# Kernel tuning notes

Measured on AMD Instinct MI355X. Metric: run time of the kernel, lower is better.

The kernel has to match this reference:

```python
import jax, jax.numpy as jnp
import numpy as np

B, S, H, E, K, NH = 2, 2048, 1024, 8, 2, 8
HD = H // NH          # head dim = 128
HQ = H // 4           # seasonal encoder width = 256
CAP = int(B * S * 1.5 * K / E)  # expert capacity = 1536


def setup_inputs() -> dict:
    key = jax.random.key(0)
    ks = iter(jax.random.split(key, 32))

    def lin(shape):
        fan_in = shape[0]
        return jax.random.normal(next(ks), shape, jnp.float32) / np.sqrt(fan_in)

    inp = {
        "hidden_states": jax.random.normal(next(ks), (B, S, H), jnp.float32),
        # position embedding table [sequence_length, H]
        "pos_emb": jax.random.normal(next(ks), (S, H), jnp.float32) * 0.02,
        # temporal_encoder: Linear(H+2,H) -> ReLU -> Linear(H,H)
        "We1": lin((H + 2, H)), "be1": jnp.zeros((H,), jnp.float32),
        "We2": lin((H, H)),     "be2": jnp.zeros((H,), jnp.float32),
        # seasonal_encoder: Linear(1,H//4) -> ReLU -> Linear(H//4,H//4)
        "Ws1": lin((1, HQ)),   "bs1": jnp.zeros((HQ,), jnp.float32),
        "Ws2": lin((HQ, HQ)),  "bs2": jnp.zeros((HQ,), jnp.float32),
        # temporal_attention (MultiheadAttention, 8 heads)
        "Wq": lin((H, H)), "bq": jnp.zeros((H,), jnp.float32),
        "Wk": lin((H, H)), "bk": jnp.zeros((H,), jnp.float32),
        "Wv": lin((H, H)), "bv": jnp.zeros((H,), jnp.float32),
        "Wo": lin((H, H)), "bo": jnp.zeros((H,), jnp.float32),
        # temporal_router: Linear(H,H) -> ReLU -> Linear(H,E)
        "Wr1": lin((H, H)), "br1": jnp.zeros((H,), jnp.float32),
        "Wr2": lin((H, E)), "br2": jnp.zeros((E,), jnp.float32),
    }
    return inp


def _forward(hidden_states, pos_emb, We1, be1, We2, be2, Ws1, bs1, Ws2, bs2,
             Wq, bq, Wk, bk, Wv, bv, Wo, bo, Wr1, br1, Wr2, br2):
    b, s, h = hidden_states.shape
    # time features (time_info is None -> defaults)
    t = jnp.arange(s, dtype=jnp.float32)                   # [S]
    season = jnp.sin(t * 2.0 * jnp.pi / 24.0)              # [S]
    time_feat = jnp.broadcast_to(jnp.stack([t, season], -1), (b, s, 2))

    combined = jnp.concatenate([hidden_states, time_feat], axis=-1)  # [B,S,H+2]
    enc = jax.nn.relu(combined @ We1 + be1) @ We2 + be2              # [B,S,H]

    pos = pos_emb[:s]                                                # [S,H]
    seas = jax.nn.relu(season[:, None] @ Ws1 + bs1) @ Ws2 + bs2      # [S,H//4]
    seas_full = jnp.tile(seas, (1, h // seas.shape[-1]))             # [S,H] (expand to H)

    x = enc + pos[None] + seas_full[None]                            # [B,S,H]

    # self-attention (eval mode, no dropout)
    def heads(y):
        return y.reshape(b, s, NH, HD)
    q = heads(x @ Wq + bq)
    k = heads(x @ Wk + bk)
    v = heads(x @ Wv + bv)
    scores = jnp.einsum('bqhd,bkhd->bhqk', q, k) / np.sqrt(HD)
    attn = jax.nn.softmax(scores, axis=-1)
    ctx = jnp.einsum('bhqk,bkhd->bqhd', attn, v).reshape(b, s, h)
    x = ctx @ Wo + bo

    logits = jax.nn.relu(x @ Wr1 + br1) @ Wr2 + br2                  # [B,S,E]
    probs = jax.nn.softmax(logits, axis=-1)

    topv, topi = jax.lax.top_k(probs, K)                             # [B,S,K]
    topv = topv / topv.sum(-1, keepdims=True)

    onehot = jax.nn.one_hot(topi, E, dtype=probs.dtype)              # [B,S,K,E]
    disp0 = onehot.sum(-2)                                           # [B,S,E] (0/1)
    comb0 = (topv[..., None] * onehot).sum(-2)                       # [B,S,E]

    # only capacity slot 0 is ever written (per original code)
    dispatch = jnp.zeros((b, s, E, CAP), probs.dtype).at[..., 0].set(disp0)
    combine = jnp.zeros((b, s, E, CAP), probs.dtype).at[..., 0].set(comb0)

    p_mean = probs.mean(axis=(0, 1))                                 # [E]
    aux_loss = jnp.sum(p_mean * jnp.log(p_mean * E + 1e-9))
    return dispatch, combine, probs, aux_loss


def reference(hidden_states, pos_emb, We1, be1, We2, be2, Ws1, bs1, Ws2, bs2,
              Wq, bq, Wk, bk, Wv, bv, Wo, bo, Wr1, br1, Wr2, br2):
    return _forward(hidden_states, pos_emb, We1, be1, We2, be2, Ws1, bs1, Ws2, bs2,
                    Wq, bq, Wk, bk, Wv, bv, Wo, bo, Wr1, br1, Wr2, br2)
```

## Files before the change

### kernel.cpp

```cpp
#include <hip/hip_runtime.h>
#include <hip/hip_fp16.h>
#include <math.h>

#define N_TOK 4096
#define S_LEN 2048
#define H_DIM 1024
#define E_EXP 8
#define CAPV  1536
#define NHEAD 8
#define HDHD  128

typedef __attribute__((ext_vector_type(8))) _Float16 v8h;
typedef __attribute__((ext_vector_type(4))) float v4f;

__device__ __forceinline__ void splitf16(float v, unsigned short& h, unsigned short& l) {
    __half hh = __float2half(v);
    h = __half_as_ushort(hh);
    l = __half_as_ushort(__float2half(v - __half2float(hh)));
}

__device__ __forceinline__ void gld_lds16(const void* g, void* l) {
    __builtin_amdgcn_global_load_lds(
        (const __attribute__((address_space(1))) unsigned int*)g,
        (__attribute__((address_space(3))) unsigned int*)l,
        16, 0, 0);
}

__global__ __launch_bounds__(256) void prep_k(
    const float* __restrict__ hid, unsigned short* __restrict__ hi,
    unsigned short* __restrict__ lo,
    const float* __restrict__ Ws1, const float* __restrict__ bs1,
    const float* __restrict__ Ws2, const float* __restrict__ bs2,
    float* __restrict__ seasons, float* __restrict__ seas24,
    const float* __restrict__ Wr2, float* __restrict__ wr2t) {
    __shared__ float hbuf[256];
    int blk = blockIdx.x;
    int tid = threadIdx.x;
    if (blk < 4096) {
        int i = blk * 256 + tid;
        float4 v = ((const float4*)hid)[i];
        ushort4 h, l;
        splitf16(v.x, h.x, l.x);
        splitf16(v.y, h.y, l.y);
        splitf16(v.z, h.z, l.z);
        splitf16(v.w, h.w, l.w);
        ((ushort4*)hi)[i] = h;
        ((ushort4*)lo)[i] = l;
    } else if (blk < 4104) {
        int s = (blk - 4096) * 256 + tid;
        if (s < S_LEN) {
            double a = (double)s * 2.0 * M_PI / 24.0;
            seasons[s] = (float)sin(a);
        }
    } else if (blk < 4128) {
        int m = blk - 4104;
        double a = (double)m * 2.0 * M_PI / 24.0;
        float sv = (float)sin(a);
        int j = tid;
        hbuf[j] = fmaxf(sv * Ws1[j] + bs1[j], 0.f);
        __syncthreads();
        float acc = bs2[j];
        for (int i = 0; i < 256; ++i) acc = fmaf(hbuf[i], Ws2[i * 256 + j], acc);
        seas24[m * 256 + j] = acc;
    } else {
        int i = (blk - 4128) * 256 + tid;
        int k = i >> 3, e = i & 7;
        wr2t[e * 1024 + k] = Wr2[i];
    }
}

__device__ __forceinline__ void wconv_body(const float* __restrict__ W,
                                           unsigned short* __restrict__ Thi,
                                           unsigned short* __restrict__ Tlo) {
    __shared__ unsigned short Hs[64][65];
    __shared__ unsigned short Ls[64][65];
    int k0 = blockIdx.y * 64, n0 = blockIdx.x * 64;
    int tid = threadIdx.x;
#pragma unroll
    for (int i = 0; i < 4; ++i) {
        int idx = tid + i * 256;
        int kk = idx >> 4, n4 = idx & 15;
        float4 v = *(const float4*)(W + (size_t)(k0 + kk) * 1024 + n0 + n4 * 4);
        unsigned short h, l;
        splitf16(v.x, h, l); Hs[n4 * 4 + 0][kk] = h; Ls[n4 * 4 + 0][kk] = l;
        splitf16(v.y, h, l); Hs[n4 * 4 + 1][kk] = h; Ls[n4 * 4 + 1][kk] = l;
        splitf16(v.z, h, l); Hs[n4 * 4 + 2][kk] = h; Ls[n4 * 4 + 2][kk] = l;
        splitf16(v.w, h, l); Hs[n4 * 4 + 3][kk] = h; Ls[n4 * 4 + 3][kk] = l;
    }
    __syncthreads();
#pragma unroll
    for (int i = 0; i < 4; ++i) {
        int idx = tid + i * 256;
        int n = idx >> 4, k4 = idx & 15;
        ushort4 h = make_ushort4(Hs[n][k4 * 4], Hs[n][k4 * 4 + 1], Hs[n][k4 * 4 + 2], Hs[n][k4 * 4 + 3]);
        ushort4 l = make_ushort4(Ls[n][k4 * 4], Ls[n][k4 * 4 + 1], Ls[n][k4 * 4 + 2], Ls[n][k4 * 4 + 3]);
        *(ushort4*)(Thi + (size_t)(n0 + n) * 1024 + k0 + k4 * 4) = h;
        *(ushort4*)(Tlo + (size_t)(n0 + n) * 1024 + k0 + k4 * 4) = l;
    }
}

__global__ __launch_bounds__(256) void wconv_t_k(const float* __restrict__ W,
                                                 unsigned short* __restrict__ Thi,
                                                 unsigned short* __restrict__ Tlo) {
    wconv_body(W, Thi, Tlo);
}

struct WBatch {
    const float* src[7];
    unsigned short* dh[7];
    unsigned short* dl[7];
};

__global__ __launch_bounds__(256) void wconv_batch_k(WBatch wb) {
    int i = blockIdx.z;
    wconv_body(wb.src[i], wb.dh[i], wb.dl[i]);
}

template <int MODE, int EMITF, int EMITS, int EMITT>
__global__ __launch_bounds__(256, 2) void gemm_split(
    const unsigned short* __restrict__ Ahi, const unsigned short* __restrict__ Alo,
    const unsigned short* __restrict__ WThi, const unsigned short* __restrict__ WTlo,
    const float* __restrict__ bias, float* __restrict__ Cf,
    unsigned short* __restrict__ Chi, unsigned short* __restrict__ Clo,
    const float* __restrict__ rowT, const float* __restrict__ rowS,
    const float* __restrict__ seasons, const float* __restrict__ pos,
    const float* __restrict__ seas24, float escale) {
    __shared__ unsigned short Ash[2][128 * 32];
    __shared__ unsigned short Asl[2][128 * 32];
    __shared__ unsigned short Bsh[2][64 * 32];
    __shared__ unsigned short Bsl[2][64 * 32];
    int tid = threadIdx.x;
    int lane = tid & 63, w = tid >> 6;
    int l15 = lane & 15, l16 = lane >> 4;
    int wm = (w >> 1) * 64, wn = (w & 1) * 32;

    int bid = blockIdx.x;
    int mp = (bid & 7) + ((bid >> 7) << 3);
    int np = (bid >> 3) & 15;
    int m0 = mp * 128, n0 = np * 64;

    int ac0 = w * 128 + lane;
    int ac1 = ac0 + 64;
    int bc  = w * 64 + lane;
    int ar0 = ac0 >> 2, ar1 = ac1 >> 2, bn = bc >> 2;
    size_t a_src0 = (size_t)(m0 + ar0) * 1024 + (((ac0 & 3) ^ (ar0 & 3)) * 8);
    size_t a_src1 = (size_t)(m0 + ar1) * 1024 + (((ac1 & 3) ^ (ar1 & 3)) * 8);
    size_t b_src  = (size_t)(n0 + bn) * 1024 + (((bc & 3) ^ (bn & 3)) * 8);

    int a_off[4], b_off[2];
#pragma unroll
    for (int mi = 0; mi < 4; ++mi) {
        int row = wm + mi * 16 + l15;
        a_off[mi] = row * 32 + ((l16 ^ (row & 3)) * 8);
    }
#pragma unroll
    for (int ni = 0; ni < 2; ++ni) {
        int n = wn + ni * 16 + l15;
        b_off[ni] = n * 32 + ((l16 ^ (n & 3)) * 8);
    }

    auto STAGE = [&](int buf, int k0) {
        gld_lds16(Ahi + a_src0 + k0, &Ash[buf][ac0 * 8]);
        gld_lds16(Ahi + a_src1 + k0, &Ash[buf][ac1 * 8]);
        gld_lds16(Alo + a_src0 + k0, &Asl[buf][ac0 * 8]);
        gld_lds16(Alo + a_src1 + k0, &Asl[buf][ac1 * 8]);
        gld_lds16(WThi + b_src + k0, &Bsh[buf][bc * 8]);
        gld_lds16(WTlo + b_src + k0, &Bsl[buf][bc * 8]);
    };

    v4f acc[4][2] = {};
    STAGE(0, 0);
    __syncthreads();

    for (int kk = 0; kk < 32; ++kk) {
        int cur = kk & 1;
        if (kk < 31) STAGE(cur ^ 1, (kk + 1) * 32);
        v8h ah[4], al[4], bh[2], bl[2];
#pragma unroll
        for (int mi = 0; mi < 4; ++mi) {
            ah[mi] = *(const v8h*)&Ash[cur][a_off[mi]];
            al[mi] = *(const v8h*)&Asl[cur][a_off[mi]];
        }
#pragma unroll
        for (int ni = 0; ni < 2; ++ni) {
            bh[ni] = *(const v8h*)&Bsh[cur][b_off[ni]];
            bl[ni] = *(const v8h*)&Bsl[cur][b_off[ni]];
        }
#pragma unroll
        for (int mi = 0; mi < 4; ++mi)
#pragma unroll
            for (int ni = 0; ni < 2; ++ni) {
                acc[mi][ni] = __builtin_amdgcn_mfma_f32_16x16x32_f16(ah[mi], bh[ni], acc[mi][ni], 0, 0, 0);
                acc[mi][ni] = __builtin_amdgcn_mfma_f32_16x16x32_f16(al[mi], bh[ni], acc[mi][ni], 0, 0, 0);
                acc[mi][ni] = __builtin_amdgcn_mfma_f32_16x16x32_f16(ah[mi], bl[ni], acc[mi][ni], 0, 0, 0);
            }
        __syncthreads();
    }

    if (EMITT) {
#pragma unroll
        for (int mi = 0; mi < 4; ++mi) {
            int row0 = m0 + wm + mi * 16 + l16 * 4;
            int bb = row0 >> 11, ss = row0 & 2047;
#pragma unroll
            for (int ni = 0; ni < 2; ++ni) {
                int col = n0 + wn + ni * 16 + l15;
                int hh = col >> 7, dd = col & 127;
                size_t base = ((size_t)((bb * 8 + hh) * 128 + dd)) * 2048 + ss;
                ushort4 vh, vl;
                float v0 = acc[mi][ni][0] + bias[col];
                float v1 = acc[mi][ni][1] + bias[col];
                float v2 = acc[mi][ni][2] + bias[col];
                float v3 = acc[mi][ni][3] + bias[col];
                splitf16(v0, vh.x, vl.x);
                splitf16(v1, vh.y, vl.y);
                splitf16(v2, vh.z, vl.z);
                splitf16(v3, vh.w, vl.w);
                *(ushort4*)(Chi + base) = vh;
                *(ushort4*)(Clo + base) = vl;
            }
        }
    } else {
#pragma unroll
        for (int mi = 0; mi < 4; ++mi) {
#pragma unroll
            for (int r = 0; r < 4; ++r) {
                int row = m0 + wm + mi * 16 + l16 * 4 + r;
                int s = row & (S_LEN - 1);
                float tval = 0.f, seval = 0.f;
                if (MODE == 1) { tval = (float)s; seval = seasons[s]; }
#pragma unroll
                for (int ni = 0; ni < 2; ++ni) {
                    int col = n0 + wn + ni * 16 + l15;
                    float v = acc[mi][ni][r] + bias[col];
                    if (MODE == 1) v += tval * rowT[col] + seval * rowS[col];
                    if (MODE == 2) v += pos[(size_t)s * 1024 + col] + seas24[(s % 24) * 256 + (col & 255)];
                    if (MODE == 1 || MODE == 3) v = fmaxf(v, 0.f);
                    size_t o = (size_t)row * 1024 + col;
                    if (EMITF) Cf[o] = v;
                    if (EMITS) {
                        unsigned short hu, lu;
                        splitf16(v * escale, hu, lu);
                        Chi[o] = hu; Clo[o] = lu;
                    }
                }
            }
        }
    }
}

__global__ __launch_bounds__(256, 4) void attn_mfma_k(
    const unsigned short* __restrict__ qhi, const unsigned short* __restrict__ qlo,
    const unsigned short* __restrict__ khi, const unsigned short* __restrict__ klo,
    const unsigned short* __restrict__ vthi, const unsigned short* __restrict__ vtlo,
    float* __restrict__ OP, float* __restrict__ ML) {
    __shared__ unsigned short Ks_hi[32 * 128];
    __shared__ unsigned short Ks_lo[32 * 128];
    __shared__ unsigned short Vs_hi[128 * 32];
    __shared__ unsigned short Vs_lo[128 * 32];
    __shared__ unsigned int   Ps[64 * 32];

    int p = blockIdx.x;
    int x = (p >> 3) & 31;
    int g = (p & 7) + ((p >> 8) << 3);
    int bh = g >> 1, z = g & 1;
    int b = bh >> 3, h = bh & 7;
    int q0 = x * 64;
    int tid = threadIdx.x;
    int lane = tid & 63, w = tid >> 6;
    int l15 = lane & 15, l16 = lane >> 4;
    int wm = w * 16;

    v8h qa_h[4], qa_l[4];
    {
        size_t qrow = (size_t)(b * S_LEN + q0 + wm + l15) * H_DIM + h * HDHD;
#pragma unroll
        for (int ks = 0; ks < 4; ++ks) {
            qa_h[ks] = *(const v8h*)(qhi + qrow + ks * 32 + l16 * 8);
            qa_l[ks] = *(const v8h*)(qlo + qrow + ks * 32 + l16 * 8);
        }
    }

    int ktok1 = tid >> 4, kslot1 = tid & 15;
    int ktok2 = ktok1 + 16;
    size_t ksrc1 = (size_t)(b * S_LEN + ktok1) * H_DIM + h * HDHD + ((kslot1 ^ (ktok1 & 7)) * 8);
    size_t ksrc2 = (size_t)(b * S_LEN + ktok2) * H_DIM + h * HDHD + ((kslot1 ^ (ktok2 & 7)) * 8);
    int vd1 = tid >> 2, vslot1 = tid & 3;
    int vd2 = vd1 + 64;
    size_t vsrc1 = (size_t)(bh * HDHD + vd1) * S_LEN + ((vslot1 ^ ((vd1 >> 1) & 3)) * 8);
    size_t vsrc2 = (size_t)(bh * HDHD + vd2) * S_LEN + ((vslot1 ^ ((vd2 >> 1) & 3)) * 8);

    v4f accO[8] = {};
    float mreg[4] = {-1e30f, -1e30f, -1e30f, -1e30f};
    float lreg[4] = {};

    int kt0 = z * 1024;
    for (int it = 0; it < 32; ++it) {
        int kt = kt0 + it * 32;
        __syncthreads();
        size_t koff = (size_t)kt * H_DIM;
        gld_lds16(khi + ksrc1 + koff, &Ks_hi[tid * 8]);
        gld_lds16(khi + ksrc2 + koff, &Ks_hi[(tid + 256) * 8]);
        gld_lds16(klo + ksrc1 + koff, &Ks_lo[tid * 8]);
        gld_lds16(klo + ksrc2 + koff, &Ks_lo[(tid + 256) * 8]);
        gld_lds16(vthi + vsrc1 + kt, &Vs_hi[tid * 8]);
        gld_lds16(vthi + vsrc2 + kt, &Vs_hi[(tid + 256) * 8]);
        gld_lds16(vtlo + vsrc1 + kt, &Vs_lo[tid * 8]);
        gld_lds16(vtlo + vsrc2 + kt, &Vs_lo[(tid + 256) * 8]);
        __syncthreads();

        v4f s0 = {}, s1 = {};
#pragma unroll
        for (int ks = 0; ks < 4; ++ks) {
#pragma unroll
            for (int nt = 0; nt < 2; ++nt) {
                int tok = nt * 16 + l15;
                int slot = (ks * 4 + l16) ^ (tok & 7);
                v8h bhf = *(const v8h*)&Ks_hi[tok * 128 + slot * 8];
                v8h blf = *(const v8h*)&Ks_lo[tok * 128 + slot * 8];
                v4f& ss = nt ? s1 : s0;
                ss = __builtin_amdgcn_mfma_f32_16x16x32_f16(qa_h[ks], bhf, ss, 0, 0, 0);
                ss = __builtin_amdgcn_mfma_f32_16x16x32_f16(qa_l[ks], bhf, ss, 0, 0, 0);
                ss = __builtin_amdgcn_mfma_f32_16x16x32_f16(qa_h[ks], blf, ss, 0, 0, 0);
            }
        }

        float p0[4], p1[4], alpha[4];
#pragma unroll
        for (int r = 0; r < 4; ++r) {
            float tmax = fmaxf(s0[r], s1[r]);
            tmax = fmaxf(tmax, __shfl_xor(tmax, 1));
            tmax = fmaxf(tmax, __shfl_xor(tmax, 2));
            tmax = fmaxf(tmax, __shfl_xor(tmax, 4));
            tmax = fmaxf(tmax, __shfl_xor(tmax, 8));
            float mnew = fmaxf(mreg[r], tmax);
            alpha[r] = __expf(mreg[r] - mnew);
            p0[r] = __expf(s0[r] - mnew);
            p1[r] = __expf(s1[r] - mnew);
            float lt = p0[r] + p1[r];
            lt += __shfl_xor(lt, 1);
            lt += __shfl_xor(lt, 2);
            lt += __shfl_xor(lt, 4);
            lt += __shfl_xor(lt, 8);
            lreg[r] = lreg[r] * alpha[r] + lt;
            mreg[r] = mnew;
        }
#pragma unroll
        for (int nt = 0; nt < 8; ++nt)
#pragma unroll
            for (int r = 0; r < 4; ++r) accO[nt][r] *= alpha[r];

#pragma unroll
        for (int r = 0; r < 4; ++r) {
            int qq = wm + l16 * 4 + r;
            unsigned short ph, pl;
            splitf16(p0[r], ph, pl);
            int k0i = l15;
            Ps[qq * 32 + ((((k0i >> 2) ^ (qq & 7)) << 2) | (k0i & 3))] =
                (unsigned)ph | ((unsigned)pl << 16);
            splitf16(p1[r], ph, pl);
            int k1i = 16 + l15;
            Ps[qq * 32 + ((((k1i >> 2) ^ (qq & 7)) << 2) | (k1i & 3))] =
                (unsigned)ph | ((unsigned)pl << 16);
        }

        int qq = wm + l15;
        int sA = (l16 * 2) ^ (qq & 7);
        int sB = (l16 * 2 + 1) ^ (qq & 7);
        uint4 ua = *(const uint4*)&Ps[qq * 32 + sA * 4];
        uint4 ub = *(const uint4*)&Ps[qq * 32 + sB * 4];
        uint4 ahw, alw;
        ahw.x = (ua.x & 0xffffu) | (ua.y << 16);
        ahw.y = (ua.z & 0xffffu) | (ua.w << 16);
        ahw.z = (ub.x & 0xffffu) | (ub.y << 16);
        ahw.w = (ub.z & 0xffffu) | (ub.w << 16);
        alw.x = (ua.x >> 16) | (ua.y & 0xffff0000u);
        alw.y = (ua.z >> 16) | (ua.w & 0xffff0000u);
        alw.z = (ub.x >> 16) | (ub.y & 0xffff0000u);
        alw.w = (ub.z >> 16) | (ub.w & 0xffff0000u);
        v8h pA_h = __builtin_bit_cast(v8h, ahw);
        v8h pA_l = __builtin_bit_cast(v8h, alw);
#pragma unroll
        for (int nt = 0; nt < 8; ++nt) {
            int d = nt * 16 + l15;
            int slot = l16 ^ ((d >> 1) & 3);
            v8h vhf = *(const v8h*)&Vs_hi[d * 32 + slot * 8];
            v8h vlf = *(const v8h*)&Vs_lo[d * 32 + slot * 8];
            accO[nt] = __builtin_amdgcn_mfma_f32_16x16x32_f16(pA_h, vhf, accO[nt], 0, 0, 0);
            accO[nt] = __builtin_amdgcn_mfma_f32_16x16x32_f16(pA_l, vhf, accO[nt], 0, 0, 0);
            accO[nt] = __builtin_amdgcn_mfma_f32_16x16x32_f16(pA_h, vlf, accO[nt], 0, 0, 0);
        }
    }

#pragma unroll
    for (int r = 0; r < 4; ++r) {
        if (l15 == 0) {
            int q = q0 + wm + l16 * 4 + r;
            size_t mlo = ((size_t)(z * 16 + bh) * 2048 + q) * 2;
            ML[mlo] = mreg[r];
            ML[mlo + 1] = lreg[r];
        }
    }
#pragma unroll
    for (int nt = 0; nt < 8; ++nt) {
#pragma unroll
        for (int r = 0; r < 4; ++r) {
            int q = q0 + wm + l16 * 4 + r;
            size_t o = ((size_t)(z * 16 + bh) * 2048 + q) * 128 + nt * 16 + l15;
            OP[o] = accO[nt][r];
        }
    }
}

__global__ __launch_bounds__(256) void attn_combine_k(
    const float* __restrict__ OP, const float* __restrict__ ML,
    unsigned short* __restrict__ ctx_hi, unsigned short* __restrict__ ctx_lo) {
    int tid = threadIdx.x;
    int R = blockIdx.x * 16 + (tid >> 4);
    int bh = R >> 11, q = R & 2047;
    int b = bh >> 3, h = bh & 7;
    int d0 = (tid & 15) * 8;
    size_t ml0 = ((size_t)bh * 2048 + q) * 2;
    size_t ml1 = ((size_t)(16 + bh) * 2048 + q) * 2;
    float m0 = ML[ml0], l0 = ML[ml0 + 1];
    float m1 = ML[ml1], l1 = ML[ml1 + 1];
    float m = fmaxf(m0, m1);
    float w0 = __expf(m0 - m), w1 = __expf(m1 - m);
    float inv = 1.f / (w0 * l0 + w1 * l1);
    const float* O0 = OP + ((size_t)bh * 2048 + q) * 128 + d0;
    const float* O1 = OP + ((size_t)(16 + bh) * 2048 + q) * 128 + d0;
    size_t dst = ((size_t)(b * 2048 + q)) * 1024 + h * 128 + d0;
    float4 a0 = *(const float4*)O0;
    float4 a1 = *(const float4*)(O0 + 4);
    float4 c0 = *(const float4*)O1;
    float4 c1 = *(const float4*)(O1 + 4);
    ushort4 h0, h1, lo0, lo1;
    splitf16((w0 * a0.x + w1 * c0.x) * inv, h0.x, lo0.x);
    splitf16((w0 * a0.y + w1 * c0.y) * inv, h0.y, lo0.y);
    splitf16((w0 * a0.z + w1 * c0.z) * inv, h0.z, lo0.z);
    splitf16((w0 * a0.w + w1 * c0.w) * inv, h0.w, lo0.w);
    splitf16((w0 * a1.x + w1 * c1.x) * inv, h1.x, lo1.x);
    splitf16((w0 * a1.y + w1 * c1.y) * inv, h1.y, lo1.y);
    splitf16((w0 * a1.z + w1 * c1.z) * inv, h1.z, lo1.z);
    splitf16((w0 * a1.w + w1 * c1.w) * inv, h1.w, lo1.w);
    *(ushort4*)(ctx_hi + dst) = h0;
    *(ushort4*)(ctx_hi + dst + 4) = h1;
    *(ushort4*)(ctx_lo + dst) = lo0;
    *(ushort4*)(ctx_lo + dst + 4) = lo1;
}

__global__ __launch_bounds__(256) void logits_k(const float* __restrict__ h1,
                                                const float* __restrict__ Wr2T,
                                                const float* __restrict__ br2,
                                                float* __restrict__ logits) {
    __shared__ float part[256];
    int tid = threadIdx.x;
    int tok8 = tid >> 5;
    int e = (tid >> 2) & 7;
    int ch = tid & 3;
    int tok = blockIdx.x * 8 + tok8;
    const float4* h4 = (const float4*)(h1 + (size_t)tok * 1024 + ch * 256);
    const float4* w4 = (const float4*)(Wr2T + (size_t)e * 1024 + ch * 256);
    float acc = 0.f;
#pragma unroll
    for (int i = 0; i < 64; ++i) {
        float4 a = h4[i];
        float4 bb = w4[i];
        acc = fmaf(a.x, bb.x, fmaf(a.y, bb.y, fmaf(a.z, bb.z, fmaf(a.w, bb.w, acc))));
    }
    part[tid] = acc;
    __syncthreads();
    if (ch == 0) {
        float s = part[tid] + part[tid + 1] + part[tid + 2] + part[tid + 3] + br2[e];
        logits[(size_t)tok * 8 + e] = s;
    }
}

__global__ __launch_bounds__(256) void topk_fill_k(const float* __restrict__ logits,
                                                   float* __restrict__ out) {
    int tok = blockIdx.x;
    int tid = threadIdx.x;
    float l[8], p[8];
    float mx = -1e30f;
#pragma unroll
    for (int e = 0; e < 8; ++e) { l[e] = logits[(size_t)tok * 8 + e]; mx = fmaxf(mx, l[e]); }
    float sum = 0.f;
#pragma unroll
    for (int e = 0; e < 8; ++e) { p[e] = __expf(l[e] - mx); sum += p[e]; }
    float inv = 1.f / sum;
#pragma unroll
    for (int e = 0; e < 8; ++e) p[e] *= inv;
    int i1 = 0;
#pragma unroll
    for (int e = 1; e < 8; ++e) if (p[e] > p[i1]) i1 = e;
    int i2 = -1;
#pragma unroll
    for (int e = 0; e < 8; ++e) {
        if (e == i1) continue;
        if (i2 < 0 || p[e] > p[i2]) i2 = e;
    }
    float tv = p[i1] + p[i2];
    float w1 = p[i1] / tv, w2 = p[i2] / tv;

    const size_t NEC = (size_t)N_TOK * E_EXP * CAPV;
    v4f* dbase = (v4f*)(out + (size_t)tok * E_EXP * CAPV);
    v4f* cbase = (v4f*)(out + NEC + (size_t)tok * E_EXP * CAPV);
    const int NF4 = E_EXP * CAPV / 4;
#pragma unroll
    for (int it = 0; it < NF4 / 256; ++it) {
        int f = it * 256 + tid;
        int e = f / (CAPV / 4);
        int c4 = f - e * (CAPV / 4);
        v4f dv = {0.f, 0.f, 0.f, 0.f};
        v4f cv = {0.f, 0.f, 0.f, 0.f};
        if (c4 == 0) {
            if (e == i1) { dv[0] = 1.f; cv[0] = w1; }
            else if (e == i2) { dv[0] = 1.f; cv[0] = w2; }
        }
        __builtin_nontemporal_store(dv, dbase + f);
        __builtin_nontemporal_store(cv, cbase + f);
    }
    if (tid < 2) {
        float4 pv = tid == 0 ? make_float4(p[0], p[1], p[2], p[3])
                             : make_float4(p[4], p[5], p[6], p[7]);
        ((float4*)(out + 2 * NEC + (size_t)tok * 8))[tid] = pv;
    }
}

__global__ void aux_k(const float* __restrict__ probs, float* __restrict__ out_aux) {
    __shared__ float part[256];
    int tid = threadIdx.x;
    int e = tid & 7, chunk = tid >> 3;
    float s = 0.f;
    for (int t = chunk * 128; t < (chunk + 1) * 128; ++t)
        s += probs[(size_t)t * 8 + e];
    part[tid] = s;
    __syncthreads();
    if (tid < 8) {
        float tot = 0.f;
        for (int c = 0; c < 32; ++c) tot += part[c * 8 + e];
        part[tid] = tot / (float)N_TOK;
    }
    __syncthreads();
    if (tid == 0) {
        float aux = 0.f;
        for (int e2 = 0; e2 < 8; ++e2) {
            float pm = part[e2];
            aux += pm * logf(pm * 8.f + 1e-9f);
        }
        *out_aux = aux;
    }
}

extern "C" void kernel_launch(void* const* d_in, const int* in_sizes, int n_in,
                              void* d_out, int out_size, void* d_ws, size_t ws_size,
                              hipStream_t stream) {
    const float* hid = (const float*)d_in[0];
    const float* pos = (const float*)d_in[1];
    const float* We1 = (const float*)d_in[2];
    const float* be1 = (const float*)d_in[3];
    const float* We2 = (const float*)d_in[4];
    const float* be2 = (const float*)d_in[5];
    const float* Ws1 = (const float*)d_in[6];
    const float* bs1 = (const float*)d_in[7];
    const float* Ws2 = (const float*)d_in[8];
    const float* bs2 = (const float*)d_in[9];
    const float* Wq  = (const float*)d_in[10]; const float* bq = (const float*)d_in[11];
    const float* Wk  = (const float*)d_in[12]; const float* bk = (const float*)d_in[13];
    const float* Wv  = (const float*)d_in[14]; const float* bv = (const float*)d_in[15];
    const float* Wo  = (const float*)d_in[16]; const float* bo = (const float*)d_in[17];
    const float* Wr1 = (const float*)d_in[18]; const float* br1 = (const float*)d_in[19];
    const float* Wr2 = (const float*)d_in[20]; const float* br2 = (const float*)d_in[21];

    float* out = (float*)d_out;
    char* base = (char*)d_ws;
    const size_t AC  = (size_t)N_TOK * H_DIM;
    const size_t SPC = AC * 2;
    const size_t FB  = AC * 4;
    const size_t WSZ = (size_t)1024 * 1024 * 4;

    unsigned short* B1hi = (unsigned short*)(base);
    unsigned short* B1lo = (unsigned short*)(base + SPC);
    unsigned short* B2hi = (unsigned short*)(base + FB);
    unsigned short* B2lo = (unsigned short*)(base + FB + SPC);
    unsigned short* Qhi  = (unsigned short*)(base + 2 * FB);
    unsigned short* Qlo  = (unsigned short*)(base + 2 * FB + SPC);
    unsigned short* Khi  = (unsigned short*)(base + 3 * FB);
    unsigned short* Klo  = (unsigned short*)(base + 3 * FB + SPC);
    unsigned short* VThi = (unsigned short*)(base + 4 * FB);
    unsigned short* VTlo = (unsigned short*)(base + 4 * FB + SPC);
    float* h1f = (float*)(base + 3 * FB);

    char* wbase = base + 5 * FB;
    bool batched = ws_size >= 5 * FB + 7 * WSZ + (1u << 20);
    unsigned short* Whi[7];
    unsigned short* Wlo[7];
    for (int i = 0; i < 7; ++i) {
        size_t off = batched ? (size_t)i * WSZ : 0;
        Whi[i] = (unsigned short*)(wbase + off);
        Wlo[i] = (unsigned short*)(wbase + off + WSZ / 2);
    }
    char* smalls = wbase + (batched ? 7 * WSZ : WSZ);
    float* wr2t    = (float*)smalls;
    float* seas24  = wr2t + 8192;
    float* seasons = seas24 + 6144;
    float* logits  = seasons + 2048;

    const size_t NEC = (size_t)N_TOK * E_EXP * CAPV;
    const float QSCALE = 0.08838834764831845f;

    float* OP = out;
    float* ML = out + (size_t)2 * 16 * 2048 * 128;

    dim3 blk(256);
    dim3 wg(16, 16);

    prep_k<<<4160, 256, 0, stream>>>(hid, B1hi, B1lo, Ws1, bs1, Ws2, bs2,
                                     seasons, seas24, Wr2, wr2t);

    const float* wsrc[7] = {We1, We2, Wq, Wk, Wv, Wo, Wr1};
    if (batched) {
        WBatch wb;
        for (int i = 0; i < 7; ++i) { wb.src[i] = wsrc[i]; wb.dh[i] = Whi[i]; wb.dl[i] = Wlo[i]; }
        wconv_batch_k<<<dim3(16, 16, 7), blk, 0, stream>>>(wb);
    }

    auto conv = [&](int i) {
        if (!batched) wconv_t_k<<<wg, blk, 0, stream>>>(wsrc[i], Whi[i], Wlo[i]);
    };

    conv(0);
    gemm_split<1, 0, 1, 0><<<512, blk, 0, stream>>>(B1hi, B1lo, Whi[0], Wlo[0], be1,
        nullptr, B2hi, B2lo,
        We1 + (size_t)1024 * 1024, We1 + (size_t)1025 * 1024, seasons, nullptr, nullptr, 1.f);
    conv(1);
    gemm_split<2, 0, 1, 0><<<512, blk, 0, stream>>>(B2hi, B2lo, Whi[1], Wlo[1], be2,
        nullptr, B1hi, B1lo, nullptr, nullptr, nullptr, pos, seas24, 1.f);
    conv(2);
    gemm_split<0, 0, 1, 0><<<512, blk, 0, stream>>>(B1hi, B1lo, Whi[2], Wlo[2], bq,
        nullptr, Qhi, Qlo, nullptr, nullptr, nullptr, nullptr, nullptr, QSCALE);
    conv(3);
    gemm_split<0, 0, 1, 0><<<512, blk, 0, stream>>>(B1hi, B1lo, Whi[3], Wlo[3], bk,
        nullptr, Khi, Klo, nullptr, nullptr, nullptr, nullptr, nullptr, 1.f);
    conv(4);
    gemm_split<0, 0, 0, 1><<<512, blk, 0, stream>>>(B1hi, B1lo, Whi[4], Wlo[4], bv,
        nullptr, VThi, VTlo, nullptr, nullptr, nullptr, nullptr, nullptr, 1.f);

    attn_mfma_k<<<1024, 256, 0, stream>>>(Qhi, Qlo, Khi, Klo, VThi, VTlo, OP, ML);
    attn_combine_k<<<2048, 256, 0, stream>>>(OP, ML, B2hi, B2lo);

    conv(5);
    gemm_split<0, 0, 1, 0><<<512, blk, 0, stream>>>(B2hi, B2lo, Whi[5], Wlo[5], bo,
        nullptr, B1hi, B1lo, nullptr, nullptr, nullptr, nullptr, nullptr, 1.f);
    conv(6);
    gemm_split<3, 1, 0, 0><<<512, blk, 0, stream>>>(B1hi, B1lo, Whi[6], Wlo[6], br1,
        h1f, nullptr, nullptr, nullptr, nullptr, nullptr, nullptr, nullptr, 1.f);

    logits_k<<<512, 256, 0, stream>>>(h1f, wr2t, br2, logits);
    topk_fill_k<<<4096, 256, 0, stream>>>(logits, out);
    aux_k<<<1, 256, 0, stream>>>(out + 2 * NEC, out + 2 * NEC + (size_t)N_TOK * E_EXP);
}
```

Before: 610.8 us.

## Fuse Q/K/V projections into one GEMM and split dispatch fill from scatter

Q, K and V weights are converted into one concatenated buffer, and a single gemm_qkv kernel computes all three projections over a 1536-block grid. Each block's epilogue picks Q (scaled), K or transposed V output by column tile. This replaces three separate launches and should improve machine fill. The dispatch/combine zeroing moves to a standalone streaming fill kernel, and a per-token thread kernel scatters the four non-zero entries and the probabilities. The path that converted weights one at a time when workspace was small is dropped, so the code now assumes the workspace is large enough.

```diff
diff --git a/kernel.cpp b/kernel.cpp
--- a/kernel.cpp
+++ b/kernel.cpp
@@ -99,12 +99,6 @@
     }
 }
 
-__global__ __launch_bounds__(256) void wconv_t_k(const float* __restrict__ W,
-                                                 unsigned short* __restrict__ Thi,
-                                                 unsigned short* __restrict__ Tlo) {
-    wconv_body(W, Thi, Tlo);
-}
-
 struct WBatch {
     const float* src[7];
     unsigned short* dh[7];
@@ -243,6 +237,139 @@
                         splitf16(v * escale, hu, lu);
                         Chi[o] = hu; Clo[o] = lu;
                     }
+                }
+            }
+        }
+    }
+}
+
+__global__ __launch_bounds__(256, 2) void gemm_qkv(
+    const unsigned short* __restrict__ Ahi, const unsigned short* __restrict__ Alo,
+    const unsigned short* __restrict__ WT3hi, const unsigned short* __restrict__ WT3lo,
+    const float* __restrict__ bq, const float* __restrict__ bk,
+    const float* __restrict__ bv,
+    unsigned short* __restrict__ Qhi, unsigned short* __restrict__ Qlo,
+    unsigned short* __restrict__ Khi, unsigned short* __restrict__ Klo,
+    unsigned short* __restrict__ VThi, unsigned short* __restrict__ VTlo,
+    float qscale) {
+    __shared__ unsigned short Ash[2][128 * 32];
+    __shared__ unsigned short Asl[2][128 * 32];
+    __shared__ unsigned short Bsh[2][64 * 32];
+    __shared__ unsigned short Bsl[2][64 * 32];
+    int tid = threadIdx.x;
+    int lane = tid & 63, w = tid >> 6;
+    int l15 = lane & 15, l16 = lane >> 4;
+    int wm = (w >> 1) * 64, wn = (w & 1) * 32;
+
+    int bid = blockIdx.x;
+    int t = bid >> 3;
+    int mp = (bid & 7) + (t / 48) * 8;
+    int np = t % 48;
+    int m0 = mp * 128;
+    int wn0 = np * 64;
+
+    int ac0 = w * 128 + lane;
+    int ac1 = ac0 + 64;
+    int bc  = w * 64 + lane;
+    int ar0 = ac0 >> 2, ar1 = ac1 >> 2, bn = bc >> 2;
+    size_t a_src0 = (size_t)(m0 + ar0) * 1024 + (((ac0 & 3) ^ (ar0 & 3)) * 8);
+    size_t a_src1 = (size_t)(m0 + ar1) * 1024 + (((ac1 & 3) ^ (ar1 & 3)) * 8);
+    size_t b_src  = (size_t)(wn0 + bn) * 1024 + (((bc & 3) ^ (bn & 3)) * 8);
+
+    int a_off[4], b_off[2];
+#pragma unroll
+    for (int mi = 0; mi < 4; ++mi) {
+        int row = wm + mi * 16 + l15;
+        a_off[mi] = row * 32 + ((l16 ^ (row & 3)) * 8);
+    }
+#pragma unroll
+    for (int ni = 0; ni < 2; ++ni) {
+        int n = wn + ni * 16 + l15;
+        b_off[ni] = n * 32 + ((l16 ^ (n & 3)) * 8);
+    }
+
+    auto STAGE = [&](int buf, int k0) {
+        gld_lds16(Ahi + a_src0 + k0, &Ash[buf][ac0 * 8]);
+        gld_lds16(Ahi + a_src1 + k0, &Ash[buf][ac1 * 8]);
+        gld_lds16(Alo + a_src0 + k0, &Asl[buf][ac0 * 8]);
+        gld_lds16(Alo + a_src1 + k0, &Asl[buf][ac1 * 8]);
+        gld_lds16(WT3hi + b_src + k0, &Bsh[buf][bc * 8]);
+        gld_lds16(WT3lo + b_src + k0, &Bsl[buf][bc * 8]);
+    };
+
+    v4f acc[4][2] = {};
+    STAGE(0, 0);
+    __syncthreads();
+
+    for (int kk = 0; kk < 32; ++kk) {
+        int cur = kk & 1;
+        if (kk < 31) STAGE(cur ^ 1, (kk + 1) * 32);
+        v8h ah[4], al[4], bh[2], bl[2];
+#pragma unroll
+        for (int mi = 0; mi < 4; ++mi) {
+            ah[mi] = *(const v8h*)&Ash[cur][a_off[mi]];
+            al[mi] = *(const v8h*)&Asl[cur][a_off[mi]];
+        }
+#pragma unroll
+        for (int ni = 0; ni < 2; ++ni) {
+            bh[ni] = *(const v8h*)&Bsh[cur][b_off[ni]];
+            bl[ni] = *(const v8h*)&Bsl[cur][b_off[ni]];
+        }
+#pragma unroll
+        for (int mi = 0; mi < 4; ++mi)
+#pragma unroll
+            for (int ni = 0; ni < 2; ++ni) {
+                acc[mi][ni] = __builtin_amdgcn_mfma_f32_16x16x32_f16(ah[mi], bh[ni], acc[mi][ni], 0, 0, 0);
+                acc[mi][ni] = __builtin_amdgcn_mfma_f32_16x16x32_f16(al[mi], bh[ni], acc[mi][ni], 0, 0, 0);
+                acc[mi][ni] = __builtin_amdgcn_mfma_f32_16x16x32_f16(ah[mi], bl[ni], acc[mi][ni], 0, 0, 0);
+            }
+        __syncthreads();
+    }
+
+    if (np >= 32) {
+        const float* bias = bv;
+        int n0 = (np - 32) * 64;
+#pragma unroll
+        for (int mi = 0; mi < 4; ++mi) {
+            int row0 = m0 + wm + mi * 16 + l16 * 4;
+            int bb = row0 >> 11, ss = row0 & 2047;
+#pragma unroll
+            for (int ni = 0; ni < 2; ++ni) {
+                int col = n0 + wn + ni * 16 + l15;
+                int hh = col >> 7, dd = col & 127;
+                size_t base = ((size_t)((bb * 8 + hh) * 128 + dd)) * 2048 + ss;
+                ushort4 vh, vl;
+                float v0 = acc[mi][ni][0] + bias[col];
+                float v1 = acc[mi][ni][1] + bias[col];
+                float v2 = acc[mi][ni][2] + bias[col];
+                float v3 = acc[mi][ni][3] + bias[col];
+                splitf16(v0, vh.x, vl.x);
+                splitf16(v1, vh.y, vl.y);
+                splitf16(v2, vh.z, vl.z);
+                splitf16(v3, vh.w, vl.w);
+                *(ushort4*)(VThi + base) = vh;
+                *(ushort4*)(VTlo + base) = vl;
+            }
+        }
+    } else {
+        const float* bias = np < 16 ? bq : bk;
+        unsigned short* Dhi = np < 16 ? Qhi : Khi;
+        unsigned short* Dlo = np < 16 ? Qlo : Klo;
+        float esc = np < 16 ? qscale : 1.f;
+        int n0 = (np & 15) * 64;
+#pragma unroll
+        for (int mi = 0; mi < 4; ++mi) {
+#pragma unroll
+            for (int r = 0; r < 4; ++r) {
+                int row = m0 + wm + mi * 16 + l16 * 4 + r;
+#pragma unroll
+                for (int ni = 0; ni < 2; ++ni) {
+                    int col = n0 + wn + ni * 16 + l15;
+                    float v = (acc[mi][ni][r] + bias[col]) * esc;
+                    size_t o = (size_t)row * 1024 + col;
+                    unsigned short hu, lu;
+                    splitf16(v, hu, lu);
+                    Dhi[o] = hu; Dlo[o] = lu;
                 }
             }
         }
@@ -449,6 +576,16 @@
     *(ushort4*)(ctx_lo + dst + 4) = lo1;
 }
 
+__global__ __launch_bounds__(256) void fill_k(float* __restrict__ out) {
+    size_t idx = (size_t)blockIdx.x * 256 + threadIdx.x;
+    const size_t stride = (size_t)2048 * 256;
+    v4f z = {0.f, 0.f, 0.f, 0.f};
+    v4f* o = (v4f*)out;
+#pragma unroll
+    for (int i = 0; i < 48; ++i)
+        __builtin_nontemporal_store(z, o + idx + (size_t)i * stride);
+}
+
 __global__ __launch_bounds__(256) void logits_k(const float* __restrict__ h1,
                                                 const float* __restrict__ Wr2T,
                                                 const float* __restrict__ br2,
@@ -476,10 +613,10 @@
     }
 }
 
-__global__ __launch_bounds__(256) void topk_fill_k(const float* __restrict__ logits,
-                                                   float* __restrict__ out) {
-    int tok = blockIdx.x;
-    int tid = threadIdx.x;
+__global__ __launch_bounds__(256) void topk_scatter_k(const float* __restrict__ logits,
+                                                      float* __restrict__ out) {
+    int tok = blockIdx.x * 256 + threadIdx.x;
+    if (tok >= N_TOK) return;
     float l[8], p[8];
     float mx = -1e30f;
 #pragma unroll
@@ -490,6 +627,10 @@
     float inv = 1.f / sum;
 #pragma unroll
     for (int e = 0; e < 8; ++e) p[e] *= inv;
+    const size_t NEC = (size_t)N_TOK * E_EXP * CAPV;
+    float* probs_out = out + 2 * NEC;
+#pragma unroll
+    for (int e = 0; e < 8; ++e) probs_out[(size_t)tok * 8 + e] = p[e];
     int i1 = 0;
 #pragma unroll
     for (int e = 1; e < 8; ++e) if (p[e] > p[i1]) i1 = e;
@@ -499,32 +640,12 @@
         if (e == i1) continue;
         if (i2 < 0 || p[e] > p[i2]) i2 = e;
     }
-    float tv = p[i1] + p[i2];
-    float w1 = p[i1] / tv, w2 = p[i2] / tv;
-
-    const size_t NEC = (size_t)N_TOK * E_EXP * CAPV;
-    v4f* dbase = (v4f*)(out + (size_t)tok * E_EXP * CAPV);
-    v4f* cbase = (v4f*)(out + NEC + (size_t)tok * E_EXP * CAPV);
-    const int NF4 = E_EXP * CAPV / 4;
-#pragma unroll
-    for (int it = 0; it < NF4 / 256; ++it) {
-        int f = it * 256 + tid;
-        int e = f / (CAPV / 4);
-        int c4 = f - e * (CAPV / 4);
-        v4f dv = {0.f, 0.f, 0.f, 0.f};
-        v4f cv = {0.f, 0.f, 0.f, 0.f};
-        if (c4 == 0) {
-            if (e == i1) { dv[0] = 1.f; cv[0] = w1; }
-            else if (e == i2) { dv[0] = 1.f; cv[0] = w2; }
-        }
-        __builtin_nontemporal_store(dv, dbase + f);
-        __builtin_nontemporal_store(cv, cbase + f);
-    }
-    if (tid < 2) {
-        float4 pv = tid == 0 ? make_float4(p[0], p[1], p[2], p[3])
-                             : make_float4(p[4], p[5], p[6], p[7]);
-        ((float4*)(out + 2 * NEC + (size_t)tok * 8))[tid] = pv;
-    }
+    float v1 = p[i1], v2 = p[i2], tv = v1 + v2;
+    size_t base = (size_t)tok * E_EXP * CAPV;
+    out[base + (size_t)i1 * CAPV] = 1.f;
+    out[base + (size_t)i2 * CAPV] = 1.f;
+    out[NEC + base + (size_t)i1 * CAPV] = v1 / tv;
+    out[NEC + base + (size_t)i2 * CAPV] = v2 / tv;
 }
 
 __global__ void aux_k(const float* __restrict__ probs, float* __restrict__ out_aux) {
@@ -577,7 +698,7 @@
     const size_t AC  = (size_t)N_TOK * H_DIM;
     const size_t SPC = AC * 2;
     const size_t FB  = AC * 4;
-    const size_t WSZ = (size_t)1024 * 1024 * 4;
+    const size_t MB  = (size_t)1 << 20;
 
     unsigned short* B1hi = (unsigned short*)(base);
     unsigned short* B1lo = (unsigned short*)(base + SPC);
@@ -591,16 +712,18 @@
     unsigned short* VTlo = (unsigned short*)(base + 4 * FB + SPC);
     float* h1f = (float*)(base + 3 * FB);
 
-    char* wbase = base + 5 * FB;
-    bool batched = ws_size >= 5 * FB + 7 * WSZ + (1u << 20);
-    unsigned short* Whi[7];
-    unsigned short* Wlo[7];
-    for (int i = 0; i < 7; ++i) {
-        size_t off = batched ? (size_t)i * WSZ : 0;
-        Whi[i] = (unsigned short*)(wbase + off);
-        Wlo[i] = (unsigned short*)(wbase + off + WSZ / 2);
-    }
-    char* smalls = wbase + (batched ? 7 * WSZ : WSZ);
+    char* wp = base + 5 * FB;
+    unsigned short* We1hi = (unsigned short*)(wp);
+    unsigned short* We1lo = (unsigned short*)(wp + 2 * MB);
+    unsigned short* We2hi = (unsigned short*)(wp + 4 * MB);
+    unsigned short* We2lo = (unsigned short*)(wp + 6 * MB);
+    unsigned short* QKVhi = (unsigned short*)(wp + 8 * MB);
+    unsigned short* QKVlo = (unsigned short*)(wp + 14 * MB);
+    unsigned short* Wohi  = (unsigned short*)(wp + 20 * MB);
+    unsigned short* Wolo  = (unsigned short*)(wp + 22 * MB);
+    unsigned short* Wr1hi = (unsigned short*)(wp + 24 * MB);
+    unsigned short* Wr1lo = (unsigned short*)(wp + 26 * MB);
+    char* smalls = wp + 28 * MB;
     float* wr2t    = (float*)smalls;
     float* seas24  = wr2t + 8192;
     float* seasons = seas24 + 6144;
@@ -613,50 +736,40 @@
     float* ML = out + (size_t)2 * 16 * 2048 * 128;
 
     dim3 blk(256);
-    dim3 wg(16, 16);
 
     prep_k<<<4160, 256, 0, stream>>>(hid, B1hi, B1lo, Ws1, bs1, Ws2, bs2,
                                      seasons, seas24, Wr2, wr2t);
 
-    const float* wsrc[7] = {We1, We2, Wq, Wk, Wv, Wo, Wr1};
-    if (batched) {
-        WBatch wb;
-        for (int i = 0; i < 7; ++i) { wb.src[i] = wsrc[i]; wb.dh[i] = Whi[i]; wb.dl[i] = Wlo[i]; }
-        wconv_batch_k<<<dim3(16, 16, 7), blk, 0, stream>>>(wb);
-    }
-
-    auto conv = [&](int i) {
-        if (!batched) wconv_t_k<<<wg, blk, 0, stream>>>(wsrc[i], Whi[i], Wlo[i]);
-    };
-
-    conv(0);
-    gemm_split<1, 0, 1, 0><<<512, blk, 0, stream>>>(B1hi, B1lo, Whi[0], Wlo[0], be1,
+    WBatch wb;
+    wb.src[0] = We1; wb.dh[0] = We1hi; wb.dl[0] = We1lo;
+    wb.src[1] = We2; wb.dh[1] = We2hi; wb.dl[1] = We2lo;
+    wb.src[2] = Wq;  wb.dh[2] = QKVhi;                     wb.dl[2] = QKVlo;
+    wb.src[3] = Wk;  wb.dh[3] = QKVhi + (size_t)1024 * 1024;  wb.dl[3] = QKVlo + (size_t)1024 * 1024;
+    wb.src[4] = Wv;  wb.dh[4] = QKVhi + (size_t)2048 * 1024;  wb.dl[4] = QKVlo + (size_t)2048 * 1024;
+    wb.src[5] = Wo;  wb.dh[5] = Wohi;  wb.dl[5] = Wolo;
+    wb.src[6] = Wr1; wb.dh[6] = Wr1hi; wb.dl[6] = Wr1lo;
+    wconv_batch_k<<<dim3(16, 16, 7), blk, 0, stream>>>(wb);
+
+    gemm_split<1, 0, 1, 0><<<512, blk, 0, stream>>>(B1hi, B1lo, We1hi, We1lo, be1,
         nullptr, B2hi, B2lo,
         We1 + (size_t)1024 * 1024, We1 + (size_t)1025 * 1024, seasons, nullptr, nullptr, 1.f);
-    conv(1);
-    gemm_split<2, 0, 1, 0><<<512, blk, 0, stream>>>(B2hi, B2lo, Whi[1], Wlo[1], be2,
+    gemm_split<2, 0, 1, 0><<<512, blk, 0, stream>>>(B2hi, B2lo, We2hi, We2lo, be2,
         nullptr, B1hi, B1lo, nullptr, nullptr, nullptr, pos, seas24, 1.f);
-    conv(2);
-    gemm_split<0, 0, 1, 0><<<512, blk, 0, stream>>>(B1hi, B1lo, Whi[2], Wlo[2], bq,
-        nullptr, Qhi, Qlo, nullptr, nullptr, nullptr, nullptr, nullptr, QSCALE);
-    conv(3);
-    gemm_split<0, 0, 1, 0><<<512, blk, 0, stream>>>(B1hi, B1lo, Whi[3], Wlo[3], bk,
-        nullptr, Khi, Klo, nullptr, nullptr, nullptr, nullptr, nullptr, 1.f);
-    conv(4);
-    gemm_split<0, 0, 0, 1><<<512, blk, 0, stream>>>(B1hi, B1lo, Whi[4], Wlo[4], bv,
-        nullptr, VThi, VTlo, nullptr, nullptr, nullptr, nullptr, nullptr, 1.f);
+
+    gemm_qkv<<<1536, blk, 0, stream>>>(B1hi, B1lo, QKVhi, QKVlo, bq, bk, bv,
+                                       Qhi, Qlo, Khi, Klo, VThi, VTlo, QSCALE);
 
     attn_mfma_k<<<1024, 256, 0, stream>>>(Qhi, Qlo, Khi, Klo, VThi, VTlo, OP, ML);
     attn_combine_k<<<2048, 256, 0, stream>>>(OP, ML, B2hi, B2lo);
 
-    conv(5);
-    gemm_split<0, 0, 1, 0><<<512, blk, 0, stream>>>(B2hi, B2lo, Whi[5], Wlo[5], bo,
+    fill_k<<<2048, 256, 0, stream>>>(out);
+
+    gemm_split<0, 0, 1, 0><<<512, blk, 0, stream>>>(B2hi, B2lo, Wohi, Wolo, bo,
         nullptr, B1hi, B1lo, nullptr, nullptr, nullptr, nullptr, nullptr, 1.f);
-    conv(6);
-    gemm_split<3, 1, 0, 0><<<512, blk, 0, stream>>>(B1hi, B1lo, Whi[6], Wlo[6], br1,
+    gemm_split<3, 1, 0, 0><<<512, blk, 0, stream>>>(B1hi, B1lo, Wr1hi, Wr1lo, br1,
         h1f, nullptr, nullptr, nullptr, nullptr, nullptr, nullptr, nullptr, 1.f);
 
     logits_k<<<512, 256, 0, stream>>>(h1f, wr2t, br2, logits);
-    topk_fill_k<<<4096, 256, 0, stream>>>(logits, out);
+    topk_scatter_k<<<16, 256, 0, stream>>>(logits, out);
     aux_k<<<1, 256, 0, stream>>>(out + 2 * NEC, out + 2 * NEC + (size_t)N_TOK * E_EXP);
 }
```

Measured after the change: 599.3 us. About the same (-1.9%).
